# Kernel tuning notes

Hardware: AMD Instinct MI355X
Metric: run time of the kernel (lower is better)

Reference implementation:

```python
import jax, jax.numpy as jnp
import numpy as np

N, K, D = 500_000, 256, 64  # points, prototypes, feature dim


def setup_inputs() -> dict:
    key = jax.random.key(0)
    kx, km = jax.random.split(key)
    X = jax.random.normal(kx, (N, D), dtype=jnp.float32)
    mus = jax.random.normal(km, (K, D), dtype=jnp.float32)
    return {"X": X, "mus": mus}


def reference(X, mus):
    # Faithful to vmap(lambda x: argmin(sum((mus - x)**2, axis=1)))(X),
    # but expressed with the Gram-matrix distance trick so the K*D broadcast
    # is a single GEMM instead of an O(N,K,D) elementwise intermediate.
    x_sq = jnp.sum(X * X, axis=1, keepdims=True)        # [N, 1]
    mu_sq = jnp.sum(mus * mus, axis=1)                  # [K]
    d2 = x_sq - 2.0 * (X @ mus.T) + mu_sq[None, :]      # [N, K] squared dists
    return jnp.argmin(d2, axis=1)                       # [N] int assignments
```

## Files before the change

kernel.cpp:

```cpp
#include <hip/hip_runtime.h>


#define DIM 64
#define NPROTO 256
#define NBLK 1024
#define SUBT 4
#define PPI 64
#define MARGIN 0.01f

using f32x4  = __attribute__((ext_vector_type(4))) float;
using bf16x8 = __attribute__((ext_vector_type(8))) __bf16;
using bf16x4 = __attribute__((ext_vector_type(4))) __bf16;

__device__ __forceinline__ void split2(float x, __bf16& h0, __bf16& h1) {
    h0 = (__bf16)x;
    h1 = (__bf16)(x - (float)h0);
}

__device__ __forceinline__ void stage_one(__bf16* lvl0, float4 v, int wgi) {
    bf16x4 w0, w1;
    const float xf[4] = {v.x, v.y, v.z, v.w};
#pragma unroll
    for (int e = 0; e < 4; ++e) {
        __bf16 h0, h1;
        split2(xf[e], h0, h1);
        w0[e] = h0; w1[e] = h1;
    }
    ((bf16x4*)lvl0)[wgi] = w0;
    ((bf16x4*)(lvl0 + 16 * 64))[wgi] = w1;
}

__device__ __forceinline__ float4 loadx(const float* __restrict__ X, int t,
                                        int j, int srow, int spart, int n) {
    int pr = t * PPI + j * 16 + srow;
    pr = (pr < n) ? pr : (n - 1);
    return *(const float4*)(X + (size_t)pr * DIM + spart * 4);
}

__attribute__((amdgpu_waves_per_eu(3, 4)))
__global__ void __launch_bounds__(256)
argmin_mfma_kernel(const float* __restrict__ X,
                   const float* __restrict__ mus,
                   int* __restrict__ out,
                   unsigned* __restrict__ ws_count,
                   int* __restrict__ ws_list,
                   int use_list, int n) {
    __shared__ __align__(16) __bf16 s_x[2][SUBT][2][16][64];
    __shared__ float s_musq[NPROTO];
    __shared__ float s_cb[2][SUBT][4][16];
    __shared__ float s_cb2[2][SUBT][4][16];
    __shared__ int   s_ck[2][SUBT][4][16];

    const int tid = threadIdx.x;
    const int w  = tid >> 6;
    const int l  = tid & 63;
    const int lp = l & 15;
    const int lg = l >> 4;

    {
        const float4* m4 = (const float4*)(mus + tid * DIM);
        float a0 = 0.f, a1 = 0.f, a2 = 0.f, a3 = 0.f;
#pragma unroll
        for (int q = 0; q < 16; ++q) {
            float4 v = m4[q];
            a0 = fmaf(v.x, v.x, a0); a1 = fmaf(v.y, v.y, a1);
            a2 = fmaf(v.z, v.z, a2); a3 = fmaf(v.w, v.w, a3);
        }
        s_musq[tid] = (a0 + a1) + (a2 + a3);
    }

    bf16x8 amu[4][2][2];
#pragma unroll
    for (int t = 0; t < 4; ++t) {
        const int p = w * 64 + t * 16 + lp;
#pragma unroll
        for (int h = 0; h < 2; ++h) {
            const float* src = mus + (size_t)p * DIM + h * 32 + lg * 8;
            const float4 va = *(const float4*)src;
            const float4 vb = *(const float4*)(src + 4);
            const float xs[8] = {va.x, va.y, va.z, va.w, vb.x, vb.y, vb.z, vb.w};
            bf16x8 m0, m1;
#pragma unroll
            for (int e = 0; e < 8; ++e) {
                __bf16 h0, h1;
                split2(xs[e], h0, h1);
                m0[e] = h0; m1[e] = h1;
            }
            amu[t][h][0] = m0; amu[t][h][1] = m1;
        }
    }

    const int ntiles = (n + PPI - 1) / PPI;
    const int q = ntiles / NBLK, rr = ntiles % NBLK;
    const int bid = blockIdx.x;
    const int t0  = bid * q + (bid < rr ? bid : rr);
    const int cnt = q + (bid < rr ? 1 : 0);

    const int srow = tid >> 4, spart = tid & 15;
    const int wgi = spart ^ ((srow & 7) << 1);

    float4 xn0 = loadx(X, t0, 0, srow, spart, n);
    float4 xn1 = loadx(X, t0, 1, srow, spart, n);
    float4 xn2 = loadx(X, t0, 2, srow, spart, n);
    float4 xn3 = loadx(X, t0, 3, srow, spart, n);
    stage_one(&s_x[0][0][0][srow][0], xn0, wgi);
    stage_one(&s_x[0][1][0][srow][0], xn1, wgi);
    stage_one(&s_x[0][2][0][srow][0], xn2, wgi);
    stage_one(&s_x[0][3][0][srow][0], xn3, wgi);
    __syncthreads();

    for (int it = 0; it < cnt; ++it) {
        const int tile = t0 + it;
        const int par = it & 1;
        const bool more = (it + 1 < cnt);

        if (more) {
            xn0 = loadx(X, tile + 1, 0, srow, spart, n);
            xn1 = loadx(X, tile + 1, 1, srow, spart, n);
            xn2 = loadx(X, tile + 1, 2, srow, spart, n);
            xn3 = loadx(X, tile + 1, 3, srow, spart, n);
        }

#pragma unroll
        for (int j = 0; j < SUBT; ++j) {
            bf16x8 bx[2][2];
#pragma unroll
            for (int h = 0; h < 2; ++h)
#pragma unroll
                for (int v = 0; v < 2; ++v)
                    bx[h][v] = ((const bf16x8*)&s_x[par][j][v][lp][0])
                                   [(h * 4 + lg) ^ (lp & 7)];

            f32x4 acc[4] = {{0.f, 0.f, 0.f, 0.f}, {0.f, 0.f, 0.f, 0.f},
                            {0.f, 0.f, 0.f, 0.f}, {0.f, 0.f, 0.f, 0.f}};
            constexpr int PI[3] = {0, 1, 0};
            constexpr int PJ[3] = {0, 0, 1};
#pragma unroll
            for (int pp = 0; pp < 3; ++pp)
#pragma unroll
                for (int h = 0; h < 2; ++h)
#pragma unroll
                    for (int t = 0; t < 4; ++t)
                        acc[t] = __builtin_amdgcn_mfma_f32_16x16x32_bf16(
                            amu[t][h][PI[pp]], bx[h][PJ[pp]], acc[t], 0, 0, 0);

            float b1 = 3.4e38f, b2 = 3.4e38f;
            int k1 = 0;
#pragma unroll
            for (int t = 0; t < 4; ++t)
#pragma unroll
                for (int r = 0; r < 4; ++r) {
                    const int kk = w * 64 + t * 16 + lg * 4 + r;
                    const float d2 = fmaf(-2.0f, acc[t][r], s_musq[kk]);
                    const bool lt = d2 < b1;
                    const float nb2 = lt ? b1 : fminf(d2, b2);
                    b1 = lt ? d2 : b1;
                    k1 = lt ? kk : k1;
                    b2 = nb2;
                }
#pragma unroll
            for (int m = 16; m <= 32; m <<= 1) {
                const float ob1 = __shfl_xor(b1, m);
                const float ob2 = __shfl_xor(b2, m);
                const int   ok1 = __shfl_xor(k1, m);
                const float nb2 = fminf(fmaxf(b1, ob1), fminf(b2, ob2));
                const bool take = (ob1 < b1) || (ob1 == b1 && ok1 < k1);
                b1 = take ? ob1 : b1;
                k1 = take ? ok1 : k1;
                b2 = nb2;
            }
            if (lg == 0) {
                s_cb[par][j][w][lp] = b1;
                s_cb2[par][j][w][lp] = b2;
                s_ck[par][j][w][lp] = k1;
            }
        }

        if (more) {
            stage_one(&s_x[par ^ 1][0][0][srow][0], xn0, wgi);
            stage_one(&s_x[par ^ 1][1][0][srow][0], xn1, wgi);
            stage_one(&s_x[par ^ 1][2][0][srow][0], xn2, wgi);
            stage_one(&s_x[par ^ 1][3][0][srow][0], xn3, wgi);
        }

        __syncthreads();

        if (tid < PPI) {
            const int j = tid >> 4, c = tid & 15;
            float f1 = s_cb[par][j][0][c], f2 = s_cb2[par][j][0][c];
            int fk = s_ck[par][j][0][c];
#pragma unroll
            for (int ww = 1; ww < 4; ++ww) {
                const float ob1 = s_cb[par][j][ww][c];
                const float ob2 = s_cb2[par][j][ww][c];
                const int   ok1 = s_ck[par][j][ww][c];
                const float nb2 = fminf(fmaxf(f1, ob1), fminf(f2, ob2));
                if (ob1 < f1) { f1 = ob1; fk = ok1; }
                f2 = nb2;
            }
            const int i = tile * PPI + tid;
            if (i < n) {
                const bool close = (f2 - f1) < MARGIN;
                if (use_list) {
                    out[i] = fk;
                    if (close) {
                        const unsigned idx = atomicAdd(ws_count, 1u);
                        ws_list[idx] = i;
                    }
                } else {
                    out[i] = (int)((unsigned)fk | (close ? 0x80000000u : 0u));
                }
            }
        }
    }
}

__device__ __forceinline__ int recompute_point(const float* __restrict__ X,
                                               const float* __restrict__ mus,
                                               int pt, int l) {
    const float4* xr = (const float4*)(X + (size_t)pt * DIM);
    float4 xv[16];
    float xa0 = 0.f, xa1 = 0.f, xa2 = 0.f, xa3 = 0.f;
#pragma unroll
    for (int qq = 0; qq < 16; ++qq) {
        xv[qq] = xr[qq];
        xa0 = fmaf(xv[qq].x, xv[qq].x, xa0);
        xa1 = fmaf(xv[qq].y, xv[qq].y, xa1);
        xa2 = fmaf(xv[qq].z, xv[qq].z, xa2);
        xa3 = fmaf(xv[qq].w, xv[qq].w, xa3);
    }
    const float xsq = (xa0 + xa1) + (xa2 + xa3);
    float b1 = 3.4e38f; int k1 = 0;
#pragma unroll
    for (int e = 0; e < 4; ++e) {
        const int p = l * 4 + e;
        const float4* mr = (const float4*)(mus + (size_t)p * DIM);
        float d0 = 0.f, d1 = 0.f, d2a = 0.f, d3 = 0.f;
        float q0 = 0.f, q1 = 0.f, q2 = 0.f, q3 = 0.f;
#pragma unroll
        for (int qq = 0; qq < 16; ++qq) {
            const float4 mv = mr[qq];
            d0 = fmaf(mv.x, xv[qq].x, d0);
            d1 = fmaf(mv.y, xv[qq].y, d1);
            d2a = fmaf(mv.z, xv[qq].z, d2a);
            d3 = fmaf(mv.w, xv[qq].w, d3);
            q0 = fmaf(mv.x, mv.x, q0);
            q1 = fmaf(mv.y, mv.y, q1);
            q2 = fmaf(mv.z, mv.z, q2);
            q3 = fmaf(mv.w, mv.w, q3);
        }
        const float dot = (d0 + d1) + (d2a + d3);
        const float msq = (q0 + q1) + (q2 + q3);
        const float dd = (xsq - 2.0f * dot) + msq;
        if (dd < b1) { b1 = dd; k1 = p; }
    }
#pragma unroll
    for (int mm = 1; mm < 64; mm <<= 1) {
        const float ob = __shfl_xor(b1, mm);
        const int ok = __shfl_xor(k1, mm);
        if (ob < b1 || (ob == b1 && ok < k1)) { b1 = ob; k1 = ok; }
    }
    return k1;
}

__global__ void __launch_bounds__(256)
fixup_list_kernel(const float* __restrict__ X, const float* __restrict__ mus,
                  const unsigned* __restrict__ ws_count,
                  const int* __restrict__ ws_list, int* __restrict__ out) {
    const int gw = (int)((blockIdx.x * blockDim.x + threadIdx.x) >> 6);
    const int l  = threadIdx.x & 63;
    const int NW = (int)((gridDim.x * blockDim.x) >> 6);
    const int nf = (int)*ws_count;
    for (int j = gw; j < nf; j += NW) {
        const int pt = ws_list[j];
        const int k1 = recompute_point(X, mus, pt, l);
        if (l == 0) out[pt] = k1;
    }
}

__global__ void __launch_bounds__(256)
fixup_scan_kernel(const float* __restrict__ X, const float* __restrict__ mus,
                  int* __restrict__ out, int n) {
    const int gw = (int)((blockIdx.x * blockDim.x + threadIdx.x) >> 6);
    const int l  = threadIdx.x & 63;
    const int NW = (int)((gridDim.x * blockDim.x) >> 6);
    const int chunk = (n + NW - 1) / NW;
    const int base = gw * chunk;
    const int end  = (base + chunk < n) ? (base + chunk) : n;
    for (int s = base; s < end; s += 64) {
        const int i = s + l;
        const int v = (i < end) ? out[i] : 0;
        const bool fl = (i < end) && ((unsigned)v & 0x80000000u);
        unsigned long long m = __ballot(fl);
        while (m) {
            const int src = (int)__ffsll((unsigned long long)m) - 1;
            m &= m - 1;
            const int pt = __shfl(i, src);
            const int k1 = recompute_point(X, mus, pt, l);
            if (l == 0) out[pt] = k1;
        }
    }
}

extern "C" void kernel_launch(void* const* d_in, const int* in_sizes, int n_in,
                              void* d_out, int out_size, void* d_ws, size_t ws_size,
                              hipStream_t stream) {
    const float* X = (const float*)d_in[0];
    const float* mus = (const float*)d_in[1];
    int* out = (int*)d_out;
    const int n = in_sizes[0] / DIM;

    unsigned* ws_count = (unsigned*)d_ws;
    int* ws_list = (int*)((char*)d_ws + 16);
    const int use_list = (ws_size >= 16 + (size_t)n * 4) ? 1 : 0;

    if (use_list) {
        hipMemsetAsync(d_ws, 0, 16, stream);
    }

    argmin_mfma_kernel<<<NBLK, 256, 0, stream>>>(X, mus, out, ws_count,
                                                 ws_list, use_list, n);
    if (use_list) {
        fixup_list_kernel<<<256, 256, 0, stream>>>(X, mus, ws_count, ws_list,
                                                   out);
    } else {
        fixup_scan_kernel<<<512, 256, 0, stream>>>(X, mus, out, n);
    }
}
```

Baseline: 92.34 us.

## Fold mu-norm bias into MFMA accumulator and use tree argmax reduction

The -0.5*||mu||^2 term is preloaded into registers and used as the initial MFMA accumulator, so the score becomes dot minus half-norm and the task turns into an argmax. This removes the per-element fma and the shared-memory reads in the epilogue. The serial top-2 scan is replaced by a pairwise tree reduction with a shorter dependency chain. The margin is halved to match the rescaled score, and the fixup kernel grid is doubled. Together these shorten the per-subtile epilogue, at the cost of more registers, and the tree's tie-breaking differs from the old sequential order.

New measurement: 88.31 us. 4.4% less time.

```diff
diff --git a/kernel.cpp b/kernel.cpp
--- a/kernel.cpp
+++ b/kernel.cpp
@@ -6,7 +6,7 @@
 #define NBLK 1024
 #define SUBT 4
 #define PPI 64
-#define MARGIN 0.01f
+#define MARGIN_ACC 0.005f
 
 using f32x4  = __attribute__((ext_vector_type(4))) float;
 using bf16x8 = __attribute__((ext_vector_type(8))) __bf16;
@@ -66,7 +66,7 @@
             a0 = fmaf(v.x, v.x, a0); a1 = fmaf(v.y, v.y, a1);
             a2 = fmaf(v.z, v.z, a2); a3 = fmaf(v.w, v.w, a3);
         }
-        s_musq[tid] = (a0 + a1) + (a2 + a3);
+        s_musq[tid] = -0.5f * ((a0 + a1) + (a2 + a3));
     }
 
     bf16x8 amu[4][2][2];
@@ -109,6 +109,14 @@
     stage_one(&s_x[0][3][0][srow][0], xn3, wgi);
     __syncthreads();
 
+    const int kbase = w * 64 + lg * 4;
+    f32x4 mh[4];
+#pragma unroll
+    for (int t = 0; t < 4; ++t)
+#pragma unroll
+        for (int r = 0; r < 4; ++r)
+            mh[t][r] = s_musq[kbase + t * 16 + r];
+
     for (int it = 0; it < cnt; ++it) {
         const int tile = t0 + it;
         const int par = it & 1;
@@ -131,12 +139,19 @@
                     bx[h][v] = ((const bf16x8*)&s_x[par][j][v][lp][0])
                                    [(h * 4 + lg) ^ (lp & 7)];
 
-            f32x4 acc[4] = {{0.f, 0.f, 0.f, 0.f}, {0.f, 0.f, 0.f, 0.f},
-                            {0.f, 0.f, 0.f, 0.f}, {0.f, 0.f, 0.f, 0.f}};
-            constexpr int PI[3] = {0, 1, 0};
-            constexpr int PJ[3] = {0, 0, 1};
-#pragma unroll
-            for (int pp = 0; pp < 3; ++pp)
+            f32x4 acc[4];
+#pragma unroll
+            for (int t = 0; t < 4; ++t)
+                acc[t] = __builtin_amdgcn_mfma_f32_16x16x32_bf16(
+                    amu[t][0][0], bx[0][0], mh[t], 0, 0, 0);
+#pragma unroll
+            for (int t = 0; t < 4; ++t)
+                acc[t] = __builtin_amdgcn_mfma_f32_16x16x32_bf16(
+                    amu[t][1][0], bx[1][0], acc[t], 0, 0, 0);
+            constexpr int PI[2] = {1, 0};
+            constexpr int PJ[2] = {0, 1};
+#pragma unroll
+            for (int pp = 0; pp < 2; ++pp)
 #pragma unroll
                 for (int h = 0; h < 2; ++h)
 #pragma unroll
@@ -144,27 +159,40 @@
                         acc[t] = __builtin_amdgcn_mfma_f32_16x16x32_bf16(
                             amu[t][h][PI[pp]], bx[h][PJ[pp]], acc[t], 0, 0, 0);
 
-            float b1 = 3.4e38f, b2 = 3.4e38f;
-            int k1 = 0;
-#pragma unroll
-            for (int t = 0; t < 4; ++t)
-#pragma unroll
-                for (int r = 0; r < 4; ++r) {
-                    const int kk = w * 64 + t * 16 + lg * 4 + r;
-                    const float d2 = fmaf(-2.0f, acc[t][r], s_musq[kk]);
-                    const bool lt = d2 < b1;
-                    const float nb2 = lt ? b1 : fminf(d2, b2);
-                    b1 = lt ? d2 : b1;
-                    k1 = lt ? kk : k1;
-                    b2 = nb2;
+            float m1[8], m2[8];
+            int   ka[8];
+#pragma unroll
+            for (int p = 0; p < 8; ++p) {
+                const int t = p >> 1, rbase = (p & 1) * 2;
+                const float da = acc[t][rbase], db = acc[t][rbase + 1];
+                const bool gt = db > da;
+                m1[p] = gt ? db : da;
+                m2[p] = gt ? da : db;
+                ka[p] = kbase + t * 16 + (gt ? rbase + 1 : rbase);
+            }
+#pragma unroll
+            for (int lvl = 0; lvl < 3; ++lvl) {
+                const int step = 1 << lvl;
+#pragma unroll
+                for (int p = 0; p < 8; p += 2 * step) {
+                    const int pb = p + step;
+                    const bool gt = m1[pb] > m1[p];
+                    const float lo = fminf(m1[p], m1[pb]);
+                    m1[p] = gt ? m1[pb] : m1[p];
+                    ka[p] = gt ? ka[pb] : ka[p];
+                    m2[p] = fmaxf(fmaxf(lo, m2[p]), m2[pb]);
                 }
+            }
+            float b1 = m1[0], b2 = m2[0];
+            int k1 = ka[0];
+
 #pragma unroll
             for (int m = 16; m <= 32; m <<= 1) {
                 const float ob1 = __shfl_xor(b1, m);
                 const float ob2 = __shfl_xor(b2, m);
                 const int   ok1 = __shfl_xor(k1, m);
-                const float nb2 = fminf(fmaxf(b1, ob1), fminf(b2, ob2));
-                const bool take = (ob1 < b1) || (ob1 == b1 && ok1 < k1);
+                const float nb2 = fmaxf(fminf(b1, ob1), fmaxf(b2, ob2));
+                const bool take = (ob1 > b1) || (ob1 == b1 && ok1 < k1);
                 b1 = take ? ob1 : b1;
                 k1 = take ? ok1 : k1;
                 b2 = nb2;
@@ -194,13 +222,13 @@
                 const float ob1 = s_cb[par][j][ww][c];
                 const float ob2 = s_cb2[par][j][ww][c];
                 const int   ok1 = s_ck[par][j][ww][c];
-                const float nb2 = fminf(fmaxf(f1, ob1), fminf(f2, ob2));
-                if (ob1 < f1) { f1 = ob1; fk = ok1; }
+                const float nb2 = fmaxf(fminf(f1, ob1), fmaxf(f2, ob2));
+                if (ob1 > f1) { f1 = ob1; fk = ok1; }
                 f2 = nb2;
             }
             const int i = tile * PPI + tid;
             if (i < n) {
-                const bool close = (f2 - f1) < MARGIN;
+                const bool close = (f1 - f2) < MARGIN_ACC;
                 if (use_list) {
                     out[i] = fk;
                     if (close) {
@@ -321,7 +349,7 @@
     argmin_mfma_kernel<<<NBLK, 256, 0, stream>>>(X, mus, out, ws_count,
                                                  ws_list, use_list, n);
     if (use_list) {
-        fixup_list_kernel<<<256, 256, 0, stream>>>(X, mus, ws_count, ws_list,
+        fixup_list_kernel<<<512, 256, 0, stream>>>(X, mus, ws_count, ws_list,
                                                    out);
     } else {
         fixup_scan_kernel<<<512, 256, 0, stream>>>(X, mus, out, n);
```
